# Performance work log

Hardware: AMD Instinct MI355X
Metric: run time of the kernel (lower is better)

Reference implementation:

```python
import jax, jax.numpy as jnp
import numpy as np


def setup_inputs() -> dict:
    key = jax.random.key(0)
    k1, k2, k3 = jax.random.split(key, 3)
    D, L, BATCH = 768, 8192, 4
    h = jax.random.normal(k1, (D, L), dtype=jnp.float32)
    x = jax.random.normal(k2, (BATCH, D, L), dtype=jnp.float32)
    B = jax.random.normal(k3, (D, 1), dtype=jnp.float32)
    return {"h": h, "x": x, "B": B}


def reference(h, x, B):
    # FFT-based long convolution (Hyena FFTConv) with residual term x * B.
    L = h.shape[-1]
    n = 2 * L  # zero-pad to 2L for linear (non-circular) convolution
    # torch.fft.rfft(..., norm='forward') divides by n; x uses default (backward, no scale);
    # torch.fft.irfft(..., norm='forward') multiplies by n. jnp supports the same norm args.
    h_f = jnp.fft.rfft(h, n=n, norm="forward")          # [D, L+1] complex
    x_f = jnp.fft.rfft(x, n=n)                            # [BATCH, D, L+1] complex
    y = jnp.fft.irfft(h_f * x_f, n=n, norm="forward")[..., :L]  # [BATCH, D, L]
    y = y + x * B  # residual with per-channel gain, B broadcasts over L
    return y.astype(h.dtype)
```

## Files before the change

### kernel.cpp

```cpp
#include <hip/hip_runtime.h>

#define DCH   768
#define NHALF 8192
#define NTH   512
#define PHYS(i) ((i) + ((i) >> 4))
#define LDSE  (NHALF + NHALF / 16)
#define NFULL 16384
#define NTH2  1024
#define LDSE2 (NFULL + NFULL / 16)

__device__ __forceinline__ float2 cmul(float2 a, float2 b) {
    return make_float2(fmaf(a.x, b.x, -(a.y * b.y)), fmaf(a.x, b.y, a.y * b.x));
}
__device__ __forceinline__ float2 cadd(float2 a, float2 b) { return make_float2(a.x + b.x, a.y + b.y); }
__device__ __forceinline__ float2 csub(float2 a, float2 b) { return make_float2(a.x - b.x, a.y - b.y); }
__device__ __forceinline__ float2 wtw(float rev) {
    return make_float2(__builtin_amdgcn_cosf(rev), __builtin_amdgcn_sinf(rev));
}
__device__ __forceinline__ int drev8(int v) {
    return ((v & 3) << 6) | ((v & 12) << 2) | ((v >> 2) & 12) | ((v >> 6) & 3);
}
__device__ __forceinline__ constexpr int rev2i(int a) { return ((a & 3) << 2) | ((a >> 2) & 3); }
__device__ __forceinline__ constexpr int rtof(int t)  { return ((t & 3) << 2) | (t >> 2); }

__device__ __forceinline__ float2 Ktw(int rt) {
    const float KC[16] = {1.0f, 0.980785280f, 0.923879533f, 0.831469612f,
                          0.707106781f, 0.555570233f, 0.382683432f, 0.195090322f,
                          0.0f, -0.195090322f, -0.382683432f, -0.555570233f,
                          -0.707106781f, -0.831469612f, -0.923879533f, -0.980785280f};
    const float KS[16] = {0.0f, -0.195090322f, -0.382683432f, -0.555570233f,
                          -0.707106781f, -0.831469612f, -0.923879533f, -0.980785280f,
                          -1.0f, -0.980785280f, -0.923879533f, -0.831469612f,
                          -0.707106781f, -0.555570233f, -0.382683432f, -0.195090322f};
    return make_float2(KC[rt], KS[rt]);
}

__device__ __forceinline__ void dif16(float2* a, float r1) {
#pragma unroll
    for (int ai = 0; ai < 4; ++ai) {
        float2 u0 = a[ai], u1 = a[ai + 4], u2 = a[ai + 8], u3 = a[ai + 12];
        float2 t0 = cadd(u0, u2), t1 = cadd(u1, u3);
        float2 t2 = csub(u0, u2), t3 = csub(u1, u3);
        float2 mi3 = make_float2(t3.y, -t3.x);
        float2 w1 = wtw(r1 - 0.0625f * ai);
        float2 w2 = cmul(w1, w1), w3 = cmul(w2, w1);
        a[ai]      = cadd(t0, t1);
        a[ai + 4]  = cmul(cadd(t2, mi3), w1);
        a[ai + 8]  = cmul(csub(t0, t1), w2);
        a[ai + 12] = cmul(csub(t2, mi3), w3);
    }
    float2 v1 = wtw(4.0f * r1);
    float2 v2 = cmul(v1, v1), v3 = cmul(v2, v1);
#pragma unroll
    for (int p = 0; p < 4; ++p) {
        float2 u0 = a[4 * p], u1 = a[4 * p + 1], u2 = a[4 * p + 2], u3 = a[4 * p + 3];
        float2 t0 = cadd(u0, u2), t1 = cadd(u1, u3);
        float2 t2 = csub(u0, u2), t3 = csub(u1, u3);
        float2 mi3 = make_float2(t3.y, -t3.x);
        a[4 * p]     = cadd(t0, t1);
        a[4 * p + 1] = cmul(cadd(t2, mi3), v1);
        a[4 * p + 2] = cmul(csub(t0, t1), v2);
        a[4 * p + 3] = cmul(csub(t2, mi3), v3);
    }
}
__device__ __forceinline__ void dit16(float2* a, float r1) {
    float2 v1 = wtw(4.0f * r1);
    float2 v2 = cmul(v1, v1), v3 = cmul(v2, v1);
#pragma unroll
    for (int p = 0; p < 4; ++p) {
        float2 b0 = a[4 * p];
        float2 b1 = cmul(a[4 * p + 1], v1);
        float2 b2 = cmul(a[4 * p + 2], v2);
        float2 b3 = cmul(a[4 * p + 3], v3);
        float2 t0 = cadd(b0, b2), t1 = csub(b0, b2);
        float2 t2 = cadd(b1, b3);
        float2 dd = csub(b3, b1);
        float2 t3 = make_float2(dd.y, -dd.x);
        a[4 * p]     = cadd(t0, t2);
        a[4 * p + 1] = cadd(t1, t3);
        a[4 * p + 2] = csub(t0, t2);
        a[4 * p + 3] = csub(t1, t3);
    }
#pragma unroll
    for (int ai = 0; ai < 4; ++ai) {
        float2 w1 = wtw(r1 + 0.0625f * ai);
        float2 w2 = cmul(w1, w1), w3 = cmul(w2, w1);
        float2 b0 = a[ai];
        float2 b1 = cmul(a[ai + 4], w1);
        float2 b2 = cmul(a[ai + 8], w2);
        float2 b3 = cmul(a[ai + 12], w3);
        float2 t0 = cadd(b0, b2), t1 = csub(b0, b2);
        float2 t2 = cadd(b1, b3);
        float2 dd = csub(b3, b1);
        float2 t3 = make_float2(dd.y, -dd.x);
        a[ai]      = cadd(t0, t2);
        a[ai + 4]  = cadd(t1, t3);
        a[ai + 8]  = csub(t0, t2);
        a[ai + 12] = csub(t1, t3);
    }
}
__device__ __forceinline__ void fwd4x4(float2* a) {
#pragma unroll
    for (int u = 0; u < 4; ++u) {
        float2 u0 = a[4*u], u1 = a[4*u+1], u2 = a[4*u+2], u3 = a[4*u+3];
        float2 t0 = cadd(u0, u2), t1 = cadd(u1, u3), t2 = csub(u0, u2), t3 = csub(u1, u3);
        float2 mi3 = make_float2(t3.y, -t3.x);
        a[4*u] = cadd(t0, t1); a[4*u+1] = cadd(t2, mi3);
        a[4*u+2] = csub(t0, t1); a[4*u+3] = csub(t2, mi3);
    }
}
__device__ __forceinline__ void inv4x4(float2* a) {
#pragma unroll
    for (int u = 0; u < 4; ++u) {
        float2 b0 = a[4*u], b1 = a[4*u+1], b2 = a[4*u+2], b3 = a[4*u+3];
        float2 t0 = cadd(b0, b2), t1 = csub(b0, b2), t2 = cadd(b1, b3);
        float2 dd = csub(b3, b1);
        float2 t3 = make_float2(dd.y, -dd.x);
        a[4*u] = cadd(t0, t2); a[4*u+1] = cadd(t1, t3);
        a[4*u+2] = csub(t0, t2); a[4*u+3] = csub(t1, t3);
    }
}

__device__ __forceinline__ void fwd8k(const float2* __restrict__ src,
                                      float2* __restrict__ z, const int w, float2* a) {
    const float R2 = 0.70710678118654752f;
#pragma unroll
    for (int g = 0; g < 2; ++g) {
        const int i0 = w + 512 * g;
        float2 c0 = src[i0], c1 = src[i0 + 1024], c2 = src[i0 + 2048], c3 = src[i0 + 3072];
        const float2 wA  = wtw(-(float)i0 * (1.0f / 8192.0f));
        const float2 wB  = cmul(wA, wA);
        const float2 wB2 = cmul(wB, wB);
        const float2 wB3 = cmul(wB2, wB);
        const int pb = PHYS(i0);
        float2 t0 = cadd(c0, c2), t1 = cadd(c1, c3), t2 = csub(c0, c2), t3 = csub(c1, c3);
        float2 mi3 = make_float2(t3.y, -t3.x);
        z[pb]            = cadd(t0, t1);
        z[pb + 1088]     = cmul(cadd(t2, mi3), wB);
        z[pb + 2 * 1088] = cmul(csub(t0, t1), wB2);
        z[pb + 3 * 1088] = cmul(csub(t2, mi3), wB3);
        float2 d0 = cmul(c0, wA);
        float2 d1 = cmul(c1, cmul(wA, make_float2(R2, -R2)));
        float2 d2 = cmul(c2, make_float2(wA.y, -wA.x));
        float2 d3 = cmul(c3, cmul(wA, make_float2(-R2, -R2)));
        t0 = cadd(d0, d2); t1 = cadd(d1, d3); t2 = csub(d0, d2); t3 = csub(d1, d3);
        mi3 = make_float2(t3.y, -t3.x);
        z[pb + 4 * 1088] = cadd(t0, t1);
        z[pb + 5 * 1088] = cmul(cadd(t2, mi3), wB);
        z[pb + 6 * 1088] = cmul(csub(t0, t1), wB2);
        z[pb + 7 * 1088] = cmul(csub(t2, mi3), wB3);
    }
    __syncthreads();
    {
        const int j = w & 63, blk = w >> 6;
        const int base = PHYS(blk * 1024 + j);
#pragma unroll
        for (int t = 0; t < 16; ++t) a[t] = z[base + 68 * t];
        dif16(a, -(float)j * (1.0f / 1024.0f));
#pragma unroll
        for (int t = 0; t < 16; ++t) z[base + 68 * t] = a[t];
    }
    __syncthreads();
    {
        const int j = w & 3, g = w >> 2;
        const int i0 = g * 64 + j;
#pragma unroll
        for (int t = 0; t < 16; ++t) a[t] = z[PHYS(i0 + 4 * t)];
        dif16(a, -(float)j * (1.0f / 64.0f));
#pragma unroll
        for (int t = 0; t < 16; ++t) z[PHYS(i0 + 4 * t)] = a[t];
    }
    __syncthreads();
    {
        const int base = 17 * w;
#pragma unroll
        for (int t = 0; t < 16; ++t) a[t] = z[base + t];
        fwd4x4(a);
#pragma unroll
        for (int t = 0; t < 16; ++t) z[base + t] = a[t];
    }
    __syncthreads();
}

extern "C" __global__ void __launch_bounds__(NTH, 4)
hspec_kernel(const float* __restrict__ hg, const float* __restrict__ bg,
             float* __restrict__ wsHf, float* __restrict__ wsNy) {
    extern __shared__ float2 z[];
    const int w = threadIdx.x;
    const int d = blockIdx.x;
    const float2* hr = (const float2*)hg + (size_t)d * 4096;
    float2 a[16];
    fwd8k(hr, z, w, a);

    const float Bd = bg[d];
    float2* out = (float2*)wsHf + (size_t)d * NHALF;
    const int wm = w & 255, whi = w >> 8;
    const int k0 = 2 * drev8(wm) + whi;
    const float2 wk0 = wtw(-(float)k0 * (1.0f / 16384.0f));
    int qm = 0;
    if (w != 0) { const int bq = (512 - k0) >> 1; qm = (whi << 8) | drev8(bq); }
#pragma unroll
    for (int t = 0; t < 16; ++t) {
        const int rt = rtof(t);
        if (w == 0 && t == 0) {
            float2 C0 = a[0];
            out[0] = make_float2(C0.x + C0.y + Bd, 0.0f);
            ((float2*)wsNy)[d] = make_float2(C0.x - C0.y + Bd, 0.0f);
        } else {
            const int cq = (w == 0) ? rev2i(16 - rt) : rev2i(15 - rt);
            const float2 Cq = z[17 * qm + cq];
            const float2 Cp = a[t];
            const float2 cA = make_float2(0.5f * (Cp.x + Cq.x), 0.5f * (Cp.y - Cq.y));
            const float2 cB = make_float2(0.5f * (Cp.y + Cq.y), -0.5f * (Cp.x - Cq.x));
            const float2 Wk = cmul(wk0, Ktw(rt));
            const float2 Hf = cadd(cA, cmul(Wk, cB));
            out[(t << 9) + w] = make_float2(Hf.x + Bd, Hf.y);
        }
    }
}

extern "C" __global__ void __launch_bounds__(NTH, 4)
fftconv_main(const float* __restrict__ xg, const float* __restrict__ wsHf,
             const float* __restrict__ wsNy, float* __restrict__ yg) {
    extern __shared__ float2 z[];
    const int w = threadIdx.x;
    const int bid = blockIdx.x;
    const int d = bid >> 2, b = bid & 3;
    const float2* xr = (const float2*)xg + (size_t)(b * DCH + d) * 4096;
    const float2* hrow = (const float2*)wsHf + (size_t)d * NHALF;
    const float R2 = 0.70710678118654752f;
    float2 a[16];
    fwd8k(xr, z, w, a);

    {
        const int wm = w & 255, whi = w >> 8;
        const int k0 = 2 * drev8(wm) + whi;
        const float2 wk0 = wtw(-(float)k0 * (1.0f / 16384.0f));
        int qm = 0;
        if (w != 0) { const int bq = (512 - k0) >> 1; qm = (whi << 8) | drev8(bq); }
#pragma unroll
        for (int t = 0; t < 16; ++t) {
            if ((t & 3) > 1) continue;
            const int rt = rtof(t);
            if (w == 0 && t == 0) {
                float2 C0 = a[0];
                float X0 = C0.x + C0.y, XN = C0.x - C0.y;
                float2 H0 = hrow[0];
                float2 HN = ((const float2*)wsNy)[d];
                float2 Y1 = make_float2(X0 * H0.x, X0 * H0.y);
                float2 Y2 = make_float2(XN * HN.x, XN * HN.y);
                float2 S  = make_float2(Y1.x + Y2.x, Y1.y - Y2.y);
                float2 Dd = make_float2(Y1.x - Y2.x, Y1.y + Y2.y);
                z[0] = make_float2(S.x - Dd.y, S.y + Dd.x);
            } else {
                const int cq = (w == 0) ? rev2i(16 - rt) : rev2i(15 - rt);
                const float2 Cq = z[17 * qm + cq];
                const float2 Cp = a[t];
                const float2 cA = make_float2(0.5f * (Cp.x + Cq.x), 0.5f * (Cp.y - Cq.y));
                const float2 cB = make_float2(0.5f * (Cp.y + Cq.y), -0.5f * (Cp.x - Cq.x));
                const float2 Wk = cmul(wk0, Ktw(rt));
                const float2 T  = cmul(Wk, cB);
                const float2 X1 = cadd(cA, T);
                const float2 X2 = make_float2(cA.x - T.x, -(cA.y - T.y));
                const float2 Hp = hrow[(t << 9) + w];
                const float2 Hq = hrow[(cq << 9) + qm];
                const float2 Y1 = cmul(X1, Hp);
                const float2 Y2 = cmul(X2, Hq);
                const float2 S  = make_float2(Y1.x + Y2.x, Y1.y - Y2.y);
                const float2 Dd = make_float2(Y1.x - Y2.x, Y1.y + Y2.y);
                const float2 Vk = make_float2(Wk.x, -Wk.y);
                const float2 U  = cmul(Vk, Dd);
                z[17 * w + t]     = make_float2(S.x - U.y, S.y + U.x);
                z[17 * qm + cq]   = make_float2(S.x + U.y, U.x - S.y);
            }
        }
        if (w == 0) {
            const float2 Cp = z[2];
            const float2 cA = make_float2(Cp.x, 0.0f);
            const float2 cB = make_float2(Cp.y, 0.0f);
            const float2 Wk = make_float2(0.0f, -1.0f);
            const float2 T  = cmul(Wk, cB);
            const float2 X1 = cadd(cA, T);
            const float2 X2 = make_float2(cA.x - T.x, -(cA.y - T.y));
            const float2 Hp = hrow[(2 << 9)];
            const float2 Y1 = cmul(X1, Hp);
            const float2 Y2 = cmul(X2, Hp);
            const float2 S  = make_float2(Y1.x + Y2.x, Y1.y - Y2.y);
            const float2 Dd = make_float2(Y1.x - Y2.x, Y1.y + Y2.y);
            const float2 Vk = make_float2(0.0f, 1.0f);
            const float2 U  = cmul(Vk, Dd);
            z[2] = make_float2(S.x - U.y, S.y + U.x);
        }
    }
    __syncthreads();
    {
        const int base = 17 * w;
#pragma unroll
        for (int t = 0; t < 16; ++t) a[t] = z[base + t];
        inv4x4(a);
#pragma unroll
        for (int t = 0; t < 16; ++t) z[base + t] = a[t];
    }
    __syncthreads();
    {
        const int j = w & 3, g = w >> 2;
        const int i0 = g * 64 + j;
#pragma unroll
        for (int t = 0; t < 16; ++t) a[t] = z[PHYS(i0 + 4 * t)];
        dit16(a, (float)j * (1.0f / 64.0f));
#pragma unroll
        for (int t = 0; t < 16; ++t) z[PHYS(i0 + 4 * t)] = a[t];
    }
    __syncthreads();
    {
        const int j = w & 63, blk = w >> 6;
        const int base = PHYS(blk * 1024 + j);
#pragma unroll
        for (int t = 0; t < 16; ++t) a[t] = z[base + 68 * t];
        dit16(a, (float)j * (1.0f / 1024.0f));
#pragma unroll
        for (int t = 0; t < 16; ++t) z[base + 68 * t] = a[t];
    }
    __syncthreads();
    {
        const float invN = 1.0f / 16384.0f;
        float2* yr = (float2*)yg + (size_t)(b * DCH + d) * 4096;
#pragma unroll
        for (int g = 0; g < 2; ++g) {
            const int i0 = w + 512 * g;
            const int pb = PHYS(i0);
            float2 q0 = z[pb],            q1 = z[pb + 1088],
                   q2 = z[pb + 2 * 1088], q3 = z[pb + 3 * 1088],
                   q4 = z[pb + 4 * 1088], q5 = z[pb + 5 * 1088],
                   q6 = z[pb + 6 * 1088], q7 = z[pb + 7 * 1088];
            const float2 vA  = wtw((float)i0 * (1.0f / 8192.0f));
            const float2 vB  = cmul(vA, vA);
            const float2 vB2 = cmul(vB, vB);
            const float2 vB3 = cmul(vB2, vB);
            float2 b1 = cmul(q1, vB), b2 = cmul(q2, vB2), b3 = cmul(q3, vB3);
            float2 t0 = cadd(q0, b2), t1 = csub(q0, b2), t2 = cadd(b1, b3);
            float2 dd = csub(b3, b1);
            float2 t3 = make_float2(dd.y, -dd.x);
            float2 T0 = cadd(t0, t2), T1 = cadd(t1, t3), T2 = csub(t0, t2), T3 = csub(t1, t3);
            b1 = cmul(q5, vB); b2 = cmul(q6, vB2); b3 = cmul(q7, vB3);
            t0 = cadd(q4, b2); t1 = csub(q4, b2); t2 = cadd(b1, b3);
            dd = csub(b3, b1);
            t3 = make_float2(dd.y, -dd.x);
            float2 B0 = cadd(t0, t2), B1 = cadd(t1, t3), B2 = csub(t0, t2), B3 = csub(t1, t3);
            float2 o0 = cadd(T0, cmul(B0, vA));
            float2 o1 = cadd(T1, cmul(B1, cmul(vA, make_float2(R2, R2))));
            float2 o2 = cadd(T2, cmul(B2, make_float2(-vA.y, vA.x)));
            float2 o3 = cadd(T3, cmul(B3, cmul(vA, make_float2(-R2, R2))));
            yr[i0]        = make_float2(o0.x * invN, o0.y * invN);
            yr[i0 + 1024] = make_float2(o1.x * invN, o1.y * invN);
            yr[i0 + 2048] = make_float2(o2.x * invN, o2.y * invN);
            yr[i0 + 3072] = make_float2(o3.x * invN, o3.y * invN);
        }
    }
}

__device__ __forceinline__ int drev14(int v) {
    int r = 0;
#pragma unroll
    for (int i = 0; i < 7; ++i) { r = (r << 2) | (v & 3); v >>= 2; }
    return r;
}
__device__ __forceinline__ int drev10(int v) {
    int r = 0;
#pragma unroll
    for (int i = 0; i < 5; ++i) { r = (r << 2) | (v & 3); v >>= 2; }
    return r;
}

extern "C" __global__ void __launch_bounds__(NTH2, 4)
fftconv_v2(const float* __restrict__ hg, const float* __restrict__ xg,
           const float* __restrict__ bg, float* __restrict__ yg) {
    extern __shared__ float2 z[];
    const int w = threadIdx.x;
    const int bid = blockIdx.x;
    const int d = bid >> 2, b = bid & 3;
    const float* xr = xg + (size_t)(b * DCH + d) * 8192;
    const float* hr = hg + (size_t)d * 8192;
    float2 a[16];
    float xv[8];
    {
#pragma unroll
        for (int t = 0; t < 8; ++t) {
            xv[t] = xr[w + 1024 * t];
            float hv = hr[w + 1024 * t];
            a[t] = make_float2(xv[t], hv);
        }
        const float r1 = -(float)w * (1.0f / 16384.0f);
#pragma unroll
        for (int ai = 0; ai < 4; ++ai) {
            float2 u0 = a[ai], u1 = a[ai + 4];
            float2 mi3 = make_float2(u1.y, -u1.x);
            float2 w1 = wtw(r1 - 0.0625f * ai);
            float2 w2 = cmul(w1, w1), w3 = cmul(w2, w1);
            a[ai]      = cadd(u0, u1);
            a[ai + 4]  = cmul(cadd(u0, mi3), w1);
            a[ai + 8]  = cmul(csub(u0, u1), w2);
            a[ai + 12] = cmul(csub(u0, mi3), w3);
        }
        float2 v1 = wtw(4.0f * r1);
        float2 v2 = cmul(v1, v1), v3 = cmul(v2, v1);
#pragma unroll
        for (int p = 0; p < 4; ++p) {
            float2 u0 = a[4 * p], u1 = a[4 * p + 1], u2 = a[4 * p + 2], u3 = a[4 * p + 3];
            float2 t0 = cadd(u0, u2), t1 = cadd(u1, u3);
            float2 t2 = csub(u0, u2), t3 = csub(u1, u3);
            float2 mi3 = make_float2(t3.y, -t3.x);
            a[4 * p]     = cadd(t0, t1);
            a[4 * p + 1] = cmul(cadd(t2, mi3), v1);
            a[4 * p + 2] = cmul(csub(t0, t1), v2);
            a[4 * p + 3] = cmul(csub(t2, mi3), v3);
        }
        const int base = PHYS(w);
#pragma unroll
        for (int t = 0; t < 16; ++t) z[base + 1088 * t] = a[t];
    }
    __syncthreads();
    {
        const int j = w & 63, grp = w >> 6;
        const int base = PHYS(grp * 1024 + j);
#pragma unroll
        for (int t = 0; t < 16; ++t) a[t] = z[base + 68 * t];
        dif16(a, -(float)j * (1.0f / 1024.0f));
#pragma unroll
        for (int t = 0; t < 16; ++t) z[base + 68 * t] = a[t];
    }
    __syncthreads();
    {
        const int j = w & 3, grp = w >> 2;
        const int i0 = grp * 64 + j;
#pragma unroll
        for (int t = 0; t < 16; ++t) a[t] = z[PHYS(i0 + 4 * t)];
        dif16(a, -(float)j * (1.0f / 64.0f));
#pragma unroll
        for (int t = 0; t < 16; ++t) z[PHYS(i0 + 4 * t)] = a[t];
    }
    __syncthreads();
    {
        const int base = 17 * w;
#pragma unroll
        for (int t = 0; t < 16; ++t) a[t] = z[base + t];
        fwd4x4(a);
#pragma unroll
        for (int t = 0; t < 16; ++t) z[base + t] = a[t];
        __syncthreads();
        const int kw = drev10(w);
#pragma unroll
        for (int t = 0; t < 16; ++t) {
            const int rt = (((t & 3) << 2) | (t >> 2));
            const int k = (rt << 10) | kw;
            const int pp = drev14(16384 - k);
            const float2 Zm = z[PHYS(pp)];
            const float2 Zp = a[t];
            const float2 A  = make_float2(Zp.x + Zm.x, Zp.y - Zm.y);
            const float2 Dv = make_float2(Zp.x - Zm.x, Zp.y + Zm.y);
            const float2 X  = make_float2(0.5f * A.x, 0.5f * A.y);
            const float2 H  = make_float2(0.5f * Dv.y, -0.5f * Dv.x);
            a[t] = cmul(X, H);
        }
        __syncthreads();
        inv4x4(a);
#pragma unroll
        for (int t = 0; t < 16; ++t) z[base + t] = a[t];
    }
    __syncthreads();
    {
        const int j = w & 3, grp = w >> 2;
        const int i0 = grp * 64 + j;
#pragma unroll
        for (int t = 0; t < 16; ++t) a[t] = z[PHYS(i0 + 4 * t)];
        dit16(a, (float)j * (1.0f / 64.0f));
#pragma unroll
        for (int t = 0; t < 16; ++t) z[PHYS(i0 + 4 * t)] = a[t];
    }
    __syncthreads();
    {
        const int j = w & 63, grp = w >> 6;
        const int base = PHYS(grp * 1024 + j);
#pragma unroll
        for (int t = 0; t < 16; ++t) a[t] = z[base + 68 * t];
        dit16(a, (float)j * (1.0f / 1024.0f));
#pragma unroll
        for (int t = 0; t < 16; ++t) z[base + 68 * t] = a[t];
    }
    __syncthreads();
    {
        const int base = PHYS(w);
#pragma unroll
        for (int t = 0; t < 16; ++t) a[t] = z[base + 1088 * t];
        const float r1 = (float)w * (1.0f / 16384.0f);
        float2 v1 = wtw(4.0f * r1);
        float2 v2 = cmul(v1, v1), v3 = cmul(v2, v1);
#pragma unroll
        for (int p = 0; p < 4; ++p) {
            float2 b0 = a[4 * p];
            float2 b1 = cmul(a[4 * p + 1], v1);
            float2 b2 = cmul(a[4 * p + 2], v2);
            float2 b3 = cmul(a[4 * p + 3], v3);
            float2 t0 = cadd(b0, b2), t1 = csub(b0, b2);
            float2 t2 = cadd(b1, b3);
            float2 dd = csub(b3, b1);
            float2 t3 = make_float2(dd.y, -dd.x);
            a[4 * p]     = cadd(t0, t2);
            a[4 * p + 1] = cadd(t1, t3);
            a[4 * p + 2] = csub(t0, t2);
            a[4 * p + 3] = csub(t1, t3);
        }
        const float bd = bg[d];
        const float invN = 1.0f / 16384.0f;
#pragma unroll
        for (int ai = 0; ai < 4; ++ai) {
            float2 w1 = wtw(r1 + 0.0625f * ai);
            float2 w2 = cmul(w1, w1), w3 = cmul(w2, w1);
            float2 b0 = a[ai];
            float2 vv1 = cmul(a[ai + 4], w1);
            float2 vv2 = cmul(a[ai + 8], w2);
            float2 vv3 = cmul(a[ai + 12], w3);
            float2 t0 = cadd(b0, vv2), t1 = csub(b0, vv2);
            float2 t2 = cadd(vv1, vv3);
            float2 dd = csub(vv3, vv1);
            float2 t3 = make_float2(dd.y, -dd.x);
            float2 o0 = cadd(t0, t2);
            float2 o1 = cadd(t1, t3);
            yg[(size_t)(b * DCH + d) * 8192 + w + 1024 * ai]        = fmaf(xv[ai], bd, o0.x * invN);
            yg[(size_t)(b * DCH + d) * 8192 + w + 4096 + 1024 * ai] = fmaf(xv[ai + 4], bd, o1.x * invN);
        }
    }
}

extern "C" void kernel_launch(void* const* d_in, const int* in_sizes, int n_in,
                              void* d_out, int out_size, void* d_ws, size_t ws_size,
                              hipStream_t stream) {
    (void)in_sizes; (void)n_in; (void)out_size;
    const float* h = (const float*)d_in[0];
    const float* x = (const float*)d_in[1];
    const float* B = (const float*)d_in[2];
    float* y = (float*)d_out;

    const size_t need = (size_t)(DCH * NHALF + DCH) * sizeof(float2);
    if (ws_size >= need && d_ws != nullptr) {
        (void)hipFuncSetAttribute((const void*)hspec_kernel,
                                  hipFuncAttributeMaxDynamicSharedMemorySize,
                                  LDSE * (int)sizeof(float2));
        (void)hipFuncSetAttribute((const void*)fftconv_main,
                                  hipFuncAttributeMaxDynamicSharedMemorySize,
                                  LDSE * (int)sizeof(float2));
        float* wsHf = (float*)d_ws;
        float* wsNy = wsHf + 2 * (size_t)DCH * NHALF;
        hspec_kernel<<<dim3(DCH), dim3(NTH), LDSE * sizeof(float2), stream>>>(h, B, wsHf, wsNy);
        fftconv_main<<<dim3(4 * DCH), dim3(NTH), LDSE * sizeof(float2), stream>>>(x, wsHf, wsNy, y);
    } else {
        (void)hipFuncSetAttribute((const void*)fftconv_v2,
                                  hipFuncAttributeMaxDynamicSharedMemorySize,
                                  LDSE2 * (int)sizeof(float2));
        fftconv_v2<<<dim3(4 * DCH), dim3(NTH2), LDSE2 * sizeof(float2), stream>>>(h, x, B, y);
    }
}
```

Before: 140.8 us.

## Use packed v2f complex math, derive twiddles by rotation, fold 1/N into spectrum

Replaces the float2 complex helpers with a 2-wide ext_vector type so the compiler can emit packed FP32 adds, muls and FMAs for the butterflies. In dif16/dit16, one sincos call now serves all twiddles, with the rest built by multiplying by constant rotations. The 1/N scale moves into the precomputed h spectrum, which drops the per-output scaling in the main kernel. This adds some rounding drift from the chained twiddle products and depends on the compiler actually choosing packed instructions.

```diff
diff --git a/kernel.cpp b/kernel.cpp
--- a/kernel.cpp
+++ b/kernel.cpp
@@ -9,13 +9,20 @@
 #define NTH2  1024
 #define LDSE2 (NFULL + NFULL / 16)
 
-__device__ __forceinline__ float2 cmul(float2 a, float2 b) {
-    return make_float2(fmaf(a.x, b.x, -(a.y * b.y)), fmaf(a.x, b.y, a.y * b.x));
-}
-__device__ __forceinline__ float2 cadd(float2 a, float2 b) { return make_float2(a.x + b.x, a.y + b.y); }
-__device__ __forceinline__ float2 csub(float2 a, float2 b) { return make_float2(a.x - b.x, a.y - b.y); }
-__device__ __forceinline__ float2 wtw(float rev) {
-    return make_float2(__builtin_amdgcn_cosf(rev), __builtin_amdgcn_sinf(rev));
+#define C1F 0.9238795325112867f
+#define S1F 0.3826834323650898f
+#define C2F 0.7071067811865476f
+
+typedef float v2f __attribute__((ext_vector_type(2)));
+
+__device__ __forceinline__ v2f mk(float x, float y) { v2f r; r.x = x; r.y = y; return r; }
+__device__ __forceinline__ v2f cmul(v2f a, v2f b) {
+    v2f re = a.xx * b;
+    return __builtin_elementwise_fma(mk(-a.y, a.y), mk(b.y, b.x), re);
+}
+__device__ __forceinline__ v2f mnegi(v2f t) { return mk(t.y, -t.x); }
+__device__ __forceinline__ v2f wtw(float rev) {
+    return mk(__builtin_amdgcn_cosf(rev), __builtin_amdgcn_sinf(rev));
 }
 __device__ __forceinline__ int drev8(int v) {
     return ((v & 3) << 6) | ((v & 12) << 2) | ((v >> 2) & 12) | ((v >> 6) & 3);
@@ -23,7 +30,7 @@
 __device__ __forceinline__ constexpr int rev2i(int a) { return ((a & 3) << 2) | ((a >> 2) & 3); }
 __device__ __forceinline__ constexpr int rtof(int t)  { return ((t & 3) << 2) | (t >> 2); }
 
-__device__ __forceinline__ float2 Ktw(int rt) {
+__device__ __forceinline__ v2f Ktw(int rt) {
     const float KC[16] = {1.0f, 0.980785280f, 0.923879533f, 0.831469612f,
                           0.707106781f, 0.555570233f, 0.382683432f, 0.195090322f,
                           0.0f, -0.195090322f, -0.382683432f, -0.555570233f,
@@ -32,123 +39,149 @@
                           -0.707106781f, -0.831469612f, -0.923879533f, -0.980785280f,
                           -1.0f, -0.980785280f, -0.923879533f, -0.831469612f,
                           -0.707106781f, -0.555570233f, -0.382683432f, -0.195090322f};
-    return make_float2(KC[rt], KS[rt]);
-}
-
-__device__ __forceinline__ void dif16(float2* a, float r1) {
+    return mk(KC[rt], KS[rt]);
+}
+
+__device__ __forceinline__ void dif16(v2f* a, float r1) {
+    const v2f w10 = wtw(r1);
+    const v2f sq  = cmul(w10, w10);
+    const v2f cu  = cmul(sq, w10);
 #pragma unroll
     for (int ai = 0; ai < 4; ++ai) {
-        float2 u0 = a[ai], u1 = a[ai + 4], u2 = a[ai + 8], u3 = a[ai + 12];
-        float2 t0 = cadd(u0, u2), t1 = cadd(u1, u3);
-        float2 t2 = csub(u0, u2), t3 = csub(u1, u3);
-        float2 mi3 = make_float2(t3.y, -t3.x);
-        float2 w1 = wtw(r1 - 0.0625f * ai);
-        float2 w2 = cmul(w1, w1), w3 = cmul(w2, w1);
-        a[ai]      = cadd(t0, t1);
-        a[ai + 4]  = cmul(cadd(t2, mi3), w1);
-        a[ai + 8]  = cmul(csub(t0, t1), w2);
-        a[ai + 12] = cmul(csub(t2, mi3), w3);
-    }
-    float2 v1 = wtw(4.0f * r1);
-    float2 v2 = cmul(v1, v1), v3 = cmul(v2, v1);
+        v2f w1, w2, w3;
+        if (ai == 0)      { w1 = w10; w2 = sq; w3 = cu; }
+        else if (ai == 1) { w1 = cmul(w10, mk(C1F, -S1F));
+                            w2 = cmul(sq,  mk(C2F, -C2F));
+                            w3 = cmul(cu,  mk(S1F, -C1F)); }
+        else if (ai == 2) { w1 = cmul(w10, mk(C2F, -C2F));
+                            w2 = mk(sq.y, -sq.x);
+                            w3 = cmul(cu,  mk(-C2F, -C2F)); }
+        else              { w1 = cmul(w10, mk(S1F, -C1F));
+                            w2 = cmul(sq,  mk(-C2F, -C2F));
+                            w3 = cmul(cu,  mk(-C1F,  S1F)); }
+        v2f u0 = a[ai], u1 = a[ai + 4], u2 = a[ai + 8], u3 = a[ai + 12];
+        v2f t0 = u0 + u2, t1 = u1 + u3;
+        v2f t2 = u0 - u2, t3 = u1 - u3;
+        v2f mi3 = mnegi(t3);
+        a[ai]      = t0 + t1;
+        a[ai + 4]  = cmul(t2 + mi3, w1);
+        a[ai + 8]  = cmul(t0 - t1, w2);
+        a[ai + 12] = cmul(t2 - mi3, w3);
+    }
+    const v2f v1 = cmul(sq, sq);
+    const v2f v2 = cmul(v1, v1);
+    const v2f v3 = cmul(v2, v1);
 #pragma unroll
     for (int p = 0; p < 4; ++p) {
-        float2 u0 = a[4 * p], u1 = a[4 * p + 1], u2 = a[4 * p + 2], u3 = a[4 * p + 3];
-        float2 t0 = cadd(u0, u2), t1 = cadd(u1, u3);
-        float2 t2 = csub(u0, u2), t3 = csub(u1, u3);
-        float2 mi3 = make_float2(t3.y, -t3.x);
-        a[4 * p]     = cadd(t0, t1);
-        a[4 * p + 1] = cmul(cadd(t2, mi3), v1);
-        a[4 * p + 2] = cmul(csub(t0, t1), v2);
-        a[4 * p + 3] = cmul(csub(t2, mi3), v3);
-    }
-}
-__device__ __forceinline__ void dit16(float2* a, float r1) {
-    float2 v1 = wtw(4.0f * r1);
-    float2 v2 = cmul(v1, v1), v3 = cmul(v2, v1);
+        v2f u0 = a[4 * p], u1 = a[4 * p + 1], u2 = a[4 * p + 2], u3 = a[4 * p + 3];
+        v2f t0 = u0 + u2, t1 = u1 + u3;
+        v2f t2 = u0 - u2, t3 = u1 - u3;
+        v2f mi3 = mnegi(t3);
+        a[4 * p]     = t0 + t1;
+        a[4 * p + 1] = cmul(t2 + mi3, v1);
+        a[4 * p + 2] = cmul(t0 - t1, v2);
+        a[4 * p + 3] = cmul(t2 - mi3, v3);
+    }
+}
+__device__ __forceinline__ void dit16(v2f* a, float r1) {
+    const v2f w10 = wtw(r1);
+    const v2f sq  = cmul(w10, w10);
+    const v2f cu  = cmul(sq, w10);
+    const v2f v1  = cmul(sq, sq);
+    const v2f v2  = cmul(v1, v1);
+    const v2f v3  = cmul(v2, v1);
 #pragma unroll
     for (int p = 0; p < 4; ++p) {
-        float2 b0 = a[4 * p];
-        float2 b1 = cmul(a[4 * p + 1], v1);
-        float2 b2 = cmul(a[4 * p + 2], v2);
-        float2 b3 = cmul(a[4 * p + 3], v3);
-        float2 t0 = cadd(b0, b2), t1 = csub(b0, b2);
-        float2 t2 = cadd(b1, b3);
-        float2 dd = csub(b3, b1);
-        float2 t3 = make_float2(dd.y, -dd.x);
-        a[4 * p]     = cadd(t0, t2);
-        a[4 * p + 1] = cadd(t1, t3);
-        a[4 * p + 2] = csub(t0, t2);
-        a[4 * p + 3] = csub(t1, t3);
+        v2f b0 = a[4 * p];
+        v2f b1 = cmul(a[4 * p + 1], v1);
+        v2f b2 = cmul(a[4 * p + 2], v2);
+        v2f b3 = cmul(a[4 * p + 3], v3);
+        v2f t0 = b0 + b2, t1 = b0 - b2;
+        v2f t2 = b1 + b3;
+        v2f dd = b3 - b1;
+        v2f t3 = mnegi(dd);
+        a[4 * p]     = t0 + t2;
+        a[4 * p + 1] = t1 + t3;
+        a[4 * p + 2] = t0 - t2;
+        a[4 * p + 3] = t1 - t3;
     }
 #pragma unroll
     for (int ai = 0; ai < 4; ++ai) {
-        float2 w1 = wtw(r1 + 0.0625f * ai);
-        float2 w2 = cmul(w1, w1), w3 = cmul(w2, w1);
-        float2 b0 = a[ai];
-        float2 b1 = cmul(a[ai + 4], w1);
-        float2 b2 = cmul(a[ai + 8], w2);
-        float2 b3 = cmul(a[ai + 12], w3);
-        float2 t0 = cadd(b0, b2), t1 = csub(b0, b2);
-        float2 t2 = cadd(b1, b3);
-        float2 dd = csub(b3, b1);
-        float2 t3 = make_float2(dd.y, -dd.x);
-        a[ai]      = cadd(t0, t2);
-        a[ai + 4]  = cadd(t1, t3);
-        a[ai + 8]  = csub(t0, t2);
-        a[ai + 12] = csub(t1, t3);
-    }
-}
-__device__ __forceinline__ void fwd4x4(float2* a) {
+        v2f w1, w2, w3;
+        if (ai == 0)      { w1 = w10; w2 = sq; w3 = cu; }
+        else if (ai == 1) { w1 = cmul(w10, mk(C1F, S1F));
+                            w2 = cmul(sq,  mk(C2F, C2F));
+                            w3 = cmul(cu,  mk(S1F, C1F)); }
+        else if (ai == 2) { w1 = cmul(w10, mk(C2F, C2F));
+                            w2 = mk(-sq.y, sq.x);
+                            w3 = cmul(cu,  mk(-C2F, C2F)); }
+        else              { w1 = cmul(w10, mk(S1F, C1F));
+                            w2 = cmul(sq,  mk(-C2F, C2F));
+                            w3 = cmul(cu,  mk(-C1F, -S1F)); }
+        v2f b0 = a[ai];
+        v2f b1 = cmul(a[ai + 4], w1);
+        v2f b2 = cmul(a[ai + 8], w2);
+        v2f b3 = cmul(a[ai + 12], w3);
+        v2f t0 = b0 + b2, t1 = b0 - b2;
+        v2f t2 = b1 + b3;
+        v2f dd = b3 - b1;
+        v2f t3 = mnegi(dd);
+        a[ai]      = t0 + t2;
+        a[ai + 4]  = t1 + t3;
+        a[ai + 8]  = t0 - t2;
+        a[ai + 12] = t1 - t3;
+    }
+}
+__device__ __forceinline__ void fwd4x4(v2f* a) {
 #pragma unroll
     for (int u = 0; u < 4; ++u) {
-        float2 u0 = a[4*u], u1 = a[4*u+1], u2 = a[4*u+2], u3 = a[4*u+3];
-        float2 t0 = cadd(u0, u2), t1 = cadd(u1, u3), t2 = csub(u0, u2), t3 = csub(u1, u3);
-        float2 mi3 = make_float2(t3.y, -t3.x);
-        a[4*u] = cadd(t0, t1); a[4*u+1] = cadd(t2, mi3);
-        a[4*u+2] = csub(t0, t1); a[4*u+3] = csub(t2, mi3);
-    }
-}
-__device__ __forceinline__ void inv4x4(float2* a) {
+        v2f u0 = a[4*u], u1 = a[4*u+1], u2 = a[4*u+2], u3 = a[4*u+3];
+        v2f t0 = u0 + u2, t1 = u1 + u3, t2 = u0 - u2, t3 = u1 - u3;
+        v2f mi3 = mnegi(t3);
+        a[4*u] = t0 + t1; a[4*u+1] = t2 + mi3;
+        a[4*u+2] = t0 - t1; a[4*u+3] = t2 - mi3;
+    }
+}
+__device__ __forceinline__ void inv4x4(v2f* a) {
 #pragma unroll
     for (int u = 0; u < 4; ++u) {
-        float2 b0 = a[4*u], b1 = a[4*u+1], b2 = a[4*u+2], b3 = a[4*u+3];
-        float2 t0 = cadd(b0, b2), t1 = csub(b0, b2), t2 = cadd(b1, b3);
-        float2 dd = csub(b3, b1);
-        float2 t3 = make_float2(dd.y, -dd.x);
-        a[4*u] = cadd(t0, t2); a[4*u+1] = cadd(t1, t3);
-        a[4*u+2] = csub(t0, t2); a[4*u+3] = csub(t1, t3);
-    }
-}
-
-__device__ __forceinline__ void fwd8k(const float2* __restrict__ src,
-                                      float2* __restrict__ z, const int w, float2* a) {
+        v2f b0 = a[4*u], b1 = a[4*u+1], b2 = a[4*u+2], b3 = a[4*u+3];
+        v2f t0 = b0 + b2, t1 = b0 - b2, t2 = b1 + b3;
+        v2f dd = b3 - b1;
+        v2f t3 = mnegi(dd);
+        a[4*u] = t0 + t2; a[4*u+1] = t1 + t3;
+        a[4*u+2] = t0 - t2; a[4*u+3] = t1 - t3;
+    }
+}
+
+__device__ __forceinline__ void fwd8k(const v2f* __restrict__ src,
+                                      v2f* __restrict__ z, const int w, v2f* a) {
     const float R2 = 0.70710678118654752f;
 #pragma unroll
     for (int g = 0; g < 2; ++g) {
         const int i0 = w + 512 * g;
-        float2 c0 = src[i0], c1 = src[i0 + 1024], c2 = src[i0 + 2048], c3 = src[i0 + 3072];
-        const float2 wA  = wtw(-(float)i0 * (1.0f / 8192.0f));
-        const float2 wB  = cmul(wA, wA);
-        const float2 wB2 = cmul(wB, wB);
-        const float2 wB3 = cmul(wB2, wB);
+        v2f c0 = src[i0], c1 = src[i0 + 1024], c2 = src[i0 + 2048], c3 = src[i0 + 3072];
+        const v2f wA  = wtw(-(float)i0 * (1.0f / 8192.0f));
+        const v2f wB  = cmul(wA, wA);
+        const v2f wB2 = cmul(wB, wB);
+        const v2f wB3 = cmul(wB2, wB);
         const int pb = PHYS(i0);
-        float2 t0 = cadd(c0, c2), t1 = cadd(c1, c3), t2 = csub(c0, c2), t3 = csub(c1, c3);
-        float2 mi3 = make_float2(t3.y, -t3.x);
-        z[pb]            = cadd(t0, t1);
-        z[pb + 1088]     = cmul(cadd(t2, mi3), wB);
-        z[pb + 2 * 1088] = cmul(csub(t0, t1), wB2);
-        z[pb + 3 * 1088] = cmul(csub(t2, mi3), wB3);
-        float2 d0 = cmul(c0, wA);
-        float2 d1 = cmul(c1, cmul(wA, make_float2(R2, -R2)));
-        float2 d2 = cmul(c2, make_float2(wA.y, -wA.x));
-        float2 d3 = cmul(c3, cmul(wA, make_float2(-R2, -R2)));
-        t0 = cadd(d0, d2); t1 = cadd(d1, d3); t2 = csub(d0, d2); t3 = csub(d1, d3);
-        mi3 = make_float2(t3.y, -t3.x);
-        z[pb + 4 * 1088] = cadd(t0, t1);
-        z[pb + 5 * 1088] = cmul(cadd(t2, mi3), wB);
-        z[pb + 6 * 1088] = cmul(csub(t0, t1), wB2);
-        z[pb + 7 * 1088] = cmul(csub(t2, mi3), wB3);
+        v2f t0 = c0 + c2, t1 = c1 + c3, t2 = c0 - c2, t3 = c1 - c3;
+        v2f mi3 = mnegi(t3);
+        z[pb]            = t0 + t1;
+        z[pb + 1088]     = cmul(t2 + mi3, wB);
+        z[pb + 2 * 1088] = cmul(t0 - t1, wB2);
+        z[pb + 3 * 1088] = cmul(t2 - mi3, wB3);
+        v2f d0 = cmul(c0, wA);
+        v2f d1 = cmul(c1, cmul(wA, mk(R2, -R2)));
+        v2f d2 = cmul(c2, mk(wA.y, -wA.x));
+        v2f d3 = cmul(c3, cmul(wA, mk(-R2, -R2)));
+        t0 = d0 + d2; t1 = d1 + d3; t2 = d0 - d2; t3 = d1 - d3;
+        mi3 = mnegi(t3);
+        z[pb + 4 * 1088] = t0 + t1;
+        z[pb + 5 * 1088] = cmul(t2 + mi3, wB);
+        z[pb + 6 * 1088] = cmul(t0 - t1, wB2);
+        z[pb + 7 * 1088] = cmul(t2 - mi3, wB3);
     }
     __syncthreads();
     {
@@ -185,36 +218,37 @@
 extern "C" __global__ void __launch_bounds__(NTH, 4)
 hspec_kernel(const float* __restrict__ hg, const float* __restrict__ bg,
              float* __restrict__ wsHf, float* __restrict__ wsNy) {
-    extern __shared__ float2 z[];
+    extern __shared__ v2f z[];
     const int w = threadIdx.x;
     const int d = blockIdx.x;
-    const float2* hr = (const float2*)hg + (size_t)d * 4096;
-    float2 a[16];
+    const v2f* hr = (const v2f*)hg + (size_t)d * 4096;
+    v2f a[16];
     fwd8k(hr, z, w, a);
 
     const float Bd = bg[d];
-    float2* out = (float2*)wsHf + (size_t)d * NHALF;
+    const float invN = 1.0f / 16384.0f;
+    v2f* out = (v2f*)wsHf + (size_t)d * NHALF;
     const int wm = w & 255, whi = w >> 8;
     const int k0 = 2 * drev8(wm) + whi;
-    const float2 wk0 = wtw(-(float)k0 * (1.0f / 16384.0f));
+    const v2f wk0 = wtw(-(float)k0 * (1.0f / 16384.0f));
     int qm = 0;
     if (w != 0) { const int bq = (512 - k0) >> 1; qm = (whi << 8) | drev8(bq); }
 #pragma unroll
     for (int t = 0; t < 16; ++t) {
         const int rt = rtof(t);
         if (w == 0 && t == 0) {
-            float2 C0 = a[0];
-            out[0] = make_float2(C0.x + C0.y + Bd, 0.0f);
-            ((float2*)wsNy)[d] = make_float2(C0.x - C0.y + Bd, 0.0f);
+            v2f C0 = a[0];
+            out[0] = mk((C0.x + C0.y + Bd) * invN, 0.0f);
+            ((v2f*)wsNy)[d] = mk((C0.x - C0.y + Bd) * invN, 0.0f);
         } else {
             const int cq = (w == 0) ? rev2i(16 - rt) : rev2i(15 - rt);
-            const float2 Cq = z[17 * qm + cq];
-            const float2 Cp = a[t];
-            const float2 cA = make_float2(0.5f * (Cp.x + Cq.x), 0.5f * (Cp.y - Cq.y));
-            const float2 cB = make_float2(0.5f * (Cp.y + Cq.y), -0.5f * (Cp.x - Cq.x));
-            const float2 Wk = cmul(wk0, Ktw(rt));
-            const float2 Hf = cadd(cA, cmul(Wk, cB));
-            out[(t << 9) + w] = make_float2(Hf.x + Bd, Hf.y);
+            const v2f Cq = z[17 * qm + cq];
+            const v2f Cp = a[t];
+            const v2f cA = mk(0.5f * (Cp.x + Cq.x), 0.5f * (Cp.y - Cq.y));
+            const v2f cB = mk(0.5f * (Cp.y + Cq.y), -0.5f * (Cp.x - Cq.x));
+            const v2f Wk = cmul(wk0, Ktw(rt));
+            const v2f Hf = cA + cmul(Wk, cB);
+            out[(t << 9) + w] = mk((Hf.x + Bd) * invN, Hf.y * invN);
         }
     }
 }
@@ -222,20 +256,20 @@
 extern "C" __global__ void __launch_bounds__(NTH, 4)
 fftconv_main(const float* __restrict__ xg, const float* __restrict__ wsHf,
              const float* __restrict__ wsNy, float* __restrict__ yg) {
-    extern __shared__ float2 z[];
+    extern __shared__ v2f z[];
     const int w = threadIdx.x;
     const int bid = blockIdx.x;
     const int d = bid >> 2, b = bid & 3;
-    const float2* xr = (const float2*)xg + (size_t)(b * DCH + d) * 4096;
-    const float2* hrow = (const float2*)wsHf + (size_t)d * NHALF;
+    const v2f* xr = (const v2f*)xg + (size_t)(b * DCH + d) * 4096;
+    const v2f* hrow = (const v2f*)wsHf + (size_t)d * NHALF;
     const float R2 = 0.70710678118654752f;
-    float2 a[16];
+    v2f a[16];
     fwd8k(xr, z, w, a);
 
     {
         const int wm = w & 255, whi = w >> 8;
         const int k0 = 2 * drev8(wm) + whi;
-        const float2 wk0 = wtw(-(float)k0 * (1.0f / 16384.0f));
+        const v2f wk0 = wtw(-(float)k0 * (1.0f / 16384.0f));
         int qm = 0;
         if (w != 0) { const int bq = (512 - k0) >> 1; qm = (whi << 8) | drev8(bq); }
 #pragma unroll
@@ -243,60 +277,61 @@
             if ((t & 3) > 1) continue;
             const int rt = rtof(t);
             if (w == 0 && t == 0) {
-                float2 C0 = a[0];
+                v2f C0 = a[0];
                 float X0 = C0.x + C0.y, XN = C0.x - C0.y;
-                float2 H0 = hrow[0];
-                float2 HN = ((const float2*)wsNy)[d];
-                float2 Y1 = make_float2(X0 * H0.x, X0 * H0.y);
-                float2 Y2 = make_float2(XN * HN.x, XN * HN.y);
-                float2 S  = make_float2(Y1.x + Y2.x, Y1.y - Y2.y);
-                float2 Dd = make_float2(Y1.x - Y2.x, Y1.y + Y2.y);
-                z[0] = make_float2(S.x - Dd.y, S.y + Dd.x);
+                v2f H0 = hrow[0];
+                v2f HN = ((const v2f*)wsNy)[d];
+                v2f Y1 = mk(X0 * H0.x, X0 * H0.y);
+                v2f Y2 = mk(XN * HN.x, XN * HN.y);
+                v2f S  = mk(Y1.x + Y2.x, Y1.y - Y2.y);
+                v2f Dd = mk(Y1.x - Y2.x, Y1.y + Y2.y);
+                a[0] = mk(S.x - Dd.y, S.y + Dd.x);
             } else {
                 const int cq = (w == 0) ? rev2i(16 - rt) : rev2i(15 - rt);
-                const float2 Cq = z[17 * qm + cq];
-                const float2 Cp = a[t];
-                const float2 cA = make_float2(0.5f * (Cp.x + Cq.x), 0.5f * (Cp.y - Cq.y));
-                const float2 cB = make_float2(0.5f * (Cp.y + Cq.y), -0.5f * (Cp.x - Cq.x));
-                const float2 Wk = cmul(wk0, Ktw(rt));
-                const float2 T  = cmul(Wk, cB);
-                const float2 X1 = cadd(cA, T);
-                const float2 X2 = make_float2(cA.x - T.x, -(cA.y - T.y));
-                const float2 Hp = hrow[(t << 9) + w];
-                const float2 Hq = hrow[(cq << 9) + qm];
-                const float2 Y1 = cmul(X1, Hp);
-                const float2 Y2 = cmul(X2, Hq);
-                const float2 S  = make_float2(Y1.x + Y2.x, Y1.y - Y2.y);
-                const float2 Dd = make_float2(Y1.x - Y2.x, Y1.y + Y2.y);
-                const float2 Vk = make_float2(Wk.x, -Wk.y);
-                const float2 U  = cmul(Vk, Dd);
-                z[17 * w + t]     = make_float2(S.x - U.y, S.y + U.x);
-                z[17 * qm + cq]   = make_float2(S.x + U.y, U.x - S.y);
+                const v2f Cq = z[17 * qm + cq];
+                const v2f Cp = a[t];
+                const v2f cA = mk(0.5f * (Cp.x + Cq.x), 0.5f * (Cp.y - Cq.y));
+                const v2f cB = mk(0.5f * (Cp.y + Cq.y), -0.5f * (Cp.x - Cq.x));
+                const v2f Wk = cmul(wk0, Ktw(rt));
+                const v2f T  = cmul(Wk, cB);
+                const v2f X1 = cA + T;
+                const v2f X2 = mk(cA.x - T.x, -(cA.y - T.y));
+                const v2f Hp = hrow[(t << 9) + w];
+                const v2f Hq = hrow[(cq << 9) + qm];
+                const v2f Y1 = cmul(X1, Hp);
+                const v2f Y2 = cmul(X2, Hq);
+                const v2f S  = mk(Y1.x + Y2.x, Y1.y - Y2.y);
+                const v2f Dd = mk(Y1.x - Y2.x, Y1.y + Y2.y);
+                const v2f Vk = mk(Wk.x, -Wk.y);
+                const v2f U  = cmul(Vk, Dd);
+                a[t]            = mk(S.x - U.y, S.y + U.x);
+                z[17 * qm + cq] = mk(S.x + U.y, U.x - S.y);
             }
         }
         if (w == 0) {
-            const float2 Cp = z[2];
-            const float2 cA = make_float2(Cp.x, 0.0f);
-            const float2 cB = make_float2(Cp.y, 0.0f);
-            const float2 Wk = make_float2(0.0f, -1.0f);
-            const float2 T  = cmul(Wk, cB);
-            const float2 X1 = cadd(cA, T);
-            const float2 X2 = make_float2(cA.x - T.x, -(cA.y - T.y));
-            const float2 Hp = hrow[(2 << 9)];
-            const float2 Y1 = cmul(X1, Hp);
-            const float2 Y2 = cmul(X2, Hp);
-            const float2 S  = make_float2(Y1.x + Y2.x, Y1.y - Y2.y);
-            const float2 Dd = make_float2(Y1.x - Y2.x, Y1.y + Y2.y);
-            const float2 Vk = make_float2(0.0f, 1.0f);
-            const float2 U  = cmul(Vk, Dd);
-            z[2] = make_float2(S.x - U.y, S.y + U.x);
+            const v2f Cp = z[2];
+            const v2f cA = mk(Cp.x, 0.0f);
+            const v2f cB = mk(Cp.y, 0.0f);
+            const v2f Wk = mk(0.0f, -1.0f);
+            const v2f T  = cmul(Wk, cB);
+            const v2f X1 = cA + T;
+            const v2f X2 = mk(cA.x - T.x, -(cA.y - T.y));
+            const v2f Hp = hrow[(2 << 9)];
+            const v2f Y1 = cmul(X1, Hp);
+            const v2f Y2 = cmul(X2, Hp);
+            const v2f S  = mk(Y1.x + Y2.x, Y1.y - Y2.y);
+            const v2f Dd = mk(Y1.x - Y2.x, Y1.y + Y2.y);
+            const v2f Vk = mk(0.0f, 1.0f);
+            const v2f U  = cmul(Vk, Dd);
+            z[2] = mk(S.x - U.y, S.y + U.x);
         }
     }
     __syncthreads();
     {
         const int base = 17 * w;
 #pragma unroll
-        for (int t = 0; t < 16; ++t) a[t] = z[base + t];
+        for (int t = 0; t < 16; ++t)
+            if ((t & 3) > 1) a[t] = z[base + t];
         inv4x4(a);
 #pragma unroll
         for (int t = 0; t < 16; ++t) z[base + t] = a[t];
@@ -323,38 +358,33 @@
     }
     __syncthreads();
     {
-        const float invN = 1.0f / 16384.0f;
-        float2* yr = (float2*)yg + (size_t)(b * DCH + d) * 4096;
+        v2f* yr = (v2f*)yg + (size_t)(b * DCH + d) * 4096;
 #pragma unroll
         for (int g = 0; g < 2; ++g) {
             const int i0 = w + 512 * g;
             const int pb = PHYS(i0);
-            float2 q0 = z[pb],            q1 = z[pb + 1088],
-                   q2 = z[pb + 2 * 1088], q3 = z[pb + 3 * 1088],
-                   q4 = z[pb + 4 * 1088], q5 = z[pb + 5 * 1088],
-                   q6 = z[pb + 6 * 1088], q7 = z[pb + 7 * 1088];
-            const float2 vA  = wtw((float)i0 * (1.0f / 8192.0f));
-            const float2 vB  = cmul(vA, vA);
-            const float2 vB2 = cmul(vB, vB);
-            const float2 vB3 = cmul(vB2, vB);
-            float2 b1 = cmul(q1, vB), b2 = cmul(q2, vB2), b3 = cmul(q3, vB3);
-            float2 t0 = cadd(q0, b2), t1 = csub(q0, b2), t2 = cadd(b1, b3);
-            float2 dd = csub(b3, b1);
-            float2 t3 = make_float2(dd.y, -dd.x);
-            float2 T0 = cadd(t0, t2), T1 = cadd(t1, t3), T2 = csub(t0, t2), T3 = csub(t1, t3);
+            v2f q0 = z[pb],            q1 = z[pb + 1088],
+                q2 = z[pb + 2 * 1088], q3 = z[pb + 3 * 1088],
+                q4 = z[pb + 4 * 1088], q5 = z[pb + 5 * 1088],
+                q6 = z[pb + 6 * 1088], q7 = z[pb + 7 * 1088];
+            const v2f vA  = wtw((float)i0 * (1.0f / 8192.0f));
+            const v2f vB  = cmul(vA, vA);
+            const v2f vB2 = cmul(vB, vB);
+            const v2f vB3 = cmul(vB2, vB);
+            v2f b1 = cmul(q1, vB), b2 = cmul(q2, vB2), b3 = cmul(q3, vB3);
+            v2f t0 = q0 + b2, t1 = q0 - b2, t2 = b1 + b3;
+            v2f dd = b3 - b1;
+            v2f t3 = mnegi(dd);
+            v2f T0 = t0 + t2, T1 = t1 + t3, T2 = t0 - t2, T3 = t1 - t3;
             b1 = cmul(q5, vB); b2 = cmul(q6, vB2); b3 = cmul(q7, vB3);
-            t0 = cadd(q4, b2); t1 = csub(q4, b2); t2 = cadd(b1, b3);
-            dd = csub(b3, b1);
-            t3 = make_float2(dd.y, -dd.x);
-            float2 B0 = cadd(t0, t2), B1 = cadd(t1, t3), B2 = csub(t0, t2), B3 = csub(t1, t3);
-            float2 o0 = cadd(T0, cmul(B0, vA));
-            float2 o1 = cadd(T1, cmul(B1, cmul(vA, make_float2(R2, R2))));
-            float2 o2 = cadd(T2, cmul(B2, make_float2(-vA.y, vA.x)));
-            float2 o3 = cadd(T3, cmul(B3, cmul(vA, make_float2(-R2, R2))));
-            yr[i0]        = make_float2(o0.x * invN, o0.y * invN);
-            yr[i0 + 1024] = make_float2(o1.x * invN, o1.y * invN);
-            yr[i0 + 2048] = make_float2(o2.x * invN, o2.y * invN);
-            yr[i0 + 3072] = make_float2(o3.x * invN, o3.y * invN);
+            t0 = q4 + b2; t1 = q4 - b2; t2 = b1 + b3;
+            dd = b3 - b1;
+            t3 = mnegi(dd);
+            v2f B0 = t0 + t2, B1 = t1 + t3, B2 = t0 - t2, B3 = t1 - t3;
+            yr[i0]        = T0 + cmul(B0, vA);
+            yr[i0 + 1024] = T1 + cmul(B1, cmul(vA, mk(R2, R2)));
+            yr[i0 + 2048] = T2 + cmul(B2, mk(-vA.y, vA.x));
+            yr[i0 + 3072] = T3 + cmul(B3, cmul(vA, mk(-R2, R2)));
         }
     }
 }
@@ -375,45 +405,45 @@
 extern "C" __global__ void __launch_bounds__(NTH2, 4)
 fftconv_v2(const float* __restrict__ hg, const float* __restrict__ xg,
            const float* __restrict__ bg, float* __restrict__ yg) {
-    extern __shared__ float2 z[];
+    extern __shared__ v2f z[];
     const int w = threadIdx.x;
     const int bid = blockIdx.x;
     const int d = bid >> 2, b = bid & 3;
     const float* xr = xg + (size_t)(b * DCH + d) * 8192;
     const float* hr = hg + (size_t)d * 8192;
-    float2 a[16];
+    v2f a[16];
     float xv[8];
     {
 #pragma unroll
         for (int t = 0; t < 8; ++t) {
             xv[t] = xr[w + 1024 * t];
             float hv = hr[w + 1024 * t];
-            a[t] = make_float2(xv[t], hv);
+            a[t] = mk(xv[t], hv);
         }
         const float r1 = -(float)w * (1.0f / 16384.0f);
 #pragma unroll
         for (int ai = 0; ai < 4; ++ai) {
-            float2 u0 = a[ai], u1 = a[ai + 4];
-            float2 mi3 = make_float2(u1.y, -u1.x);
-            float2 w1 = wtw(r1 - 0.0625f * ai);
-            float2 w2 = cmul(w1, w1), w3 = cmul(w2, w1);
-            a[ai]      = cadd(u0, u1);
-            a[ai + 4]  = cmul(cadd(u0, mi3), w1);
-            a[ai + 8]  = cmul(csub(u0, u1), w2);
-            a[ai + 12] = cmul(csub(u0, mi3), w3);
-        }
-        float2 v1 = wtw(4.0f * r1);
-        float2 v2 = cmul(v1, v1), v3 = cmul(v2, v1);
+            v2f u0 = a[ai], u1 = a[ai + 4];
+            v2f mi3 = mk(u1.y, -u1.x);
+            v2f w1 = wtw(r1 - 0.0625f * ai);
+            v2f w2 = cmul(w1, w1), w3 = cmul(w2, w1);
+            a[ai]      = u0 + u1;
+            a[ai + 4]  = cmul(u0 + mi3, w1);
+            a[ai + 8]  = cmul(u0 - u1, w2);
+            a[ai + 12] = cmul(u0 - mi3, w3);
+        }
+        v2f v1 = wtw(4.0f * r1);
+        v2f v2 = cmul(v1, v1), v3 = cmul(v2, v1);
 #pragma unroll
         for (int p = 0; p < 4; ++p) {
-            float2 u0 = a[4 * p], u1 = a[4 * p + 1], u2 = a[4 * p + 2], u3 = a[4 * p + 3];
-            float2 t0 = cadd(u0, u2), t1 = cadd(u1, u3);
-            float2 t2 = csub(u0, u2), t3 = csub(u1, u3);
-            float2 mi3 = make_float2(t3.y, -t3.x);
-            a[4 * p]     = cadd(t0, t1);
-            a[4 * p + 1] = cmul(cadd(t2, mi3), v1);
-            a[4 * p + 2] = cmul(csub(t0, t1), v2);
-            a[4 * p + 3] = cmul(csub(t2, mi3), v3);
+            v2f u0 = a[4 * p], u1 = a[4 * p + 1], u2 = a[4 * p + 2], u3 = a[4 * p + 3];
+            v2f t0 = u0 + u2, t1 = u1 + u3;
+            v2f t2 = u0 - u2, t3 = u1 - u3;
+            v2f mi3 = mnegi(t3);
+            a[4 * p]     = t0 + t1;
+            a[4 * p + 1] = cmul(t2 + mi3, v1);
+            a[4 * p + 2] = cmul(t0 - t1, v2);
+            a[4 * p + 3] = cmul(t2 - mi3, v3);
         }
         const int base = PHYS(w);
 #pragma unroll
@@ -454,12 +484,12 @@
             const int rt = (((t & 3) << 2) | (t >> 2));
             const int k = (rt << 10) | kw;
             const int pp = drev14(16384 - k);
-            const float2 Zm = z[PHYS(pp)];
-            const float2 Zp = a[t];
-            const float2 A  = make_float2(Zp.x + Zm.x, Zp.y - Zm.y);
-            const float2 Dv = make_float2(Zp.x - Zm.x, Zp.y + Zm.y);
-            const float2 X  = make_float2(0.5f * A.x, 0.5f * A.y);
-            const float2 H  = make_float2(0.5f * Dv.y, -0.5f * Dv.x);
+            const v2f Zm = z[PHYS(pp)];
+            const v2f Zp = a[t];
+            const v2f A  = mk(Zp.x + Zm.x, Zp.y - Zm.y);
+            const v2f Dv = mk(Zp.x - Zm.x, Zp.y + Zm.y);
+            const v2f X  = mk(0.5f * A.x, 0.5f * A.y);
+            const v2f H  = mk(0.5f * Dv.y, -0.5f * Dv.x);
             a[t] = cmul(X, H);
         }
         __syncthreads();
@@ -493,39 +523,39 @@
 #pragma unroll
         for (int t = 0; t < 16; ++t) a[t] = z[base + 1088 * t];
         const float r1 = (float)w * (1.0f / 16384.0f);
-        float2 v1 = wtw(4.0f * r1);
-        float2 v2 = cmul(v1, v1), v3 = cmul(v2, v1);
+        v2f v1 = wtw(4.0f * r1);
+        v2f v2 = cmul(v1, v1), v3 = cmul(v2, v1);
 #pragma unroll
         for (int p = 0; p < 4; ++p) {
-            float2 b0 = a[4 * p];
-            float2 b1 = cmul(a[4 * p + 1], v1);
-            float2 b2 = cmul(a[4 * p + 2], v2);
-            float2 b3 = cmul(a[4 * p + 3], v3);
-            float2 t0 = cadd(b0, b2), t1 = csub(b0, b2);
-            float2 t2 = cadd(b1, b3);
-            float2 dd = csub(b3, b1);
-            float2 t3 = make_float2(dd.y, -dd.x);
-            a[4 * p]     = cadd(t0, t2);
-            a[4 * p + 1] = cadd(t1, t3);
-            a[4 * p + 2] = csub(t0, t2);
-            a[4 * p + 3] = csub(t1, t3);
+            v2f b0 = a[4 * p];
+            v2f b1 = cmul(a[4 * p + 1], v1);
+            v2f b2 = cmul(a[4 * p + 2], v2);
+            v2f b3 = cmul(a[4 * p + 3], v3);
+            v2f t0 = b0 + b2, t1 = b0 - b2;
+            v2f t2 = b1 + b3;
+            v2f dd = b3 - b1;
+            v2f t3 = mnegi(dd);
+            a[4 * p]     = t0 + t2;
+            a[4 * p + 1] = t1 + t3;
+            a[4 * p + 2] = t0 - t2;
+            a[4 * p + 3] = t1 - t3;
         }
         const float bd = bg[d];
         const float invN = 1.0f / 16384.0f;
 #pragma unroll
         for (int ai = 0; ai < 4; ++ai) {
-            float2 w1 = wtw(r1 + 0.0625f * ai);
-            float2 w2 = cmul(w1, w1), w3 = cmul(w2, w1);
-            float2 b0 = a[ai];
-            float2 vv1 = cmul(a[ai + 4], w1);
-            float2 vv2 = cmul(a[ai + 8], w2);
-            float2 vv3 = cmul(a[ai + 12], w3);
-            float2 t0 = cadd(b0, vv2), t1 = csub(b0, vv2);
-            float2 t2 = cadd(vv1, vv3);
-            float2 dd = csub(vv3, vv1);
-            float2 t3 = make_float2(dd.y, -dd.x);
-            float2 o0 = cadd(t0, t2);
-            float2 o1 = cadd(t1, t3);
+            v2f w1 = wtw(r1 + 0.0625f * ai);
+            v2f w2 = cmul(w1, w1), w3 = cmul(w2, w1);
+            v2f b0 = a[ai];
+            v2f vv1 = cmul(a[ai + 4], w1);
+            v2f vv2 = cmul(a[ai + 8], w2);
+            v2f vv3 = cmul(a[ai + 12], w3);
+            v2f t0 = b0 + vv2, t1 = b0 - vv2;
+            v2f t2 = vv1 + vv3;
+            v2f dd = vv3 - vv1;
+            v2f t3 = mnegi(dd);
+            v2f o0 = t0 + t2;
+            v2f o1 = t1 + t3;
             yg[(size_t)(b * DCH + d) * 8192 + w + 1024 * ai]        = fmaf(xv[ai], bd, o0.x * invN);
             yg[(size_t)(b * DCH + d) * 8192 + w + 4096 + 1024 * ai] = fmaf(xv[ai + 4], bd, o1.x * invN);
         }
```

Result: faster. 132.0 us (median of 2 runs) (-6.2%).
